# Kernel tuning notes

Hardware: AMD Instinct MI355X
Metric: run time of the kernel (lower is better)

Reference implementation:

```python
import jax, jax.numpy as jnp
from jax import lax
import numpy as np

B, T, IN, H, L = 64, 512, 256, 512, 2


def setup_inputs() -> dict:
    key = jax.random.key(0)
    k = jax.random.split(key, 5)
    s_w = 1.0 / np.sqrt(IN)
    s_u = 1.0 / np.sqrt(H)
    return {
        "x": jax.random.normal(k[0], (B, T, IN), dtype=jnp.float32),
        "W": jax.random.uniform(k[1], (3 * H, IN), dtype=jnp.float32, minval=-s_w, maxval=s_w),
        "b_W": jax.random.uniform(k[2], (3 * H,), dtype=jnp.float32, minval=-s_w, maxval=s_w),
        "U": jax.random.uniform(k[3], (3 * H, H), dtype=jnp.float32, minval=-s_u, maxval=s_u),
        "b_U": jax.random.uniform(k[4], (3 * H,), dtype=jnp.float32, minval=-s_u, maxval=s_u),
        "num_layers": L,
    }


def _cell(xt, h, W, b_W, U, b_U):
    # xt: [B, IN], h: [B, H]
    xg = xt @ W.T + b_W          # [B, 3H]
    hg = h @ U.T + b_U           # [B, 3H]
    xr, xu, xn = jnp.split(xg, 3, axis=1)
    hr, hu, hn = jnp.split(hg, 3, axis=1)
    r = jax.nn.sigmoid(xr + hr)
    u = jax.nn.sigmoid(xu + hu)
    n = jnp.tanh(xn + r * hn)
    return u * h + (1.0 - u) * n


def reference(x, W, b_W, U, b_U, num_layers):
    b, t, _ = x.shape
    hdim = U.shape[1]

    def step(h, xt):
        hs = []
        for _ in range(num_layers):  # shared cell reapplied to same xt
            h = _cell(xt, h, W, b_W, U, b_U)
            hs.append(h)
        return h, jnp.stack(hs)      # [L, B, H]

    h0 = jnp.zeros((b, hdim), x.dtype)
    _, hs = lax.scan(step, h0, jnp.swapaxes(x, 0, 1))  # [T, L, B, H]
    return hs.reshape(t * num_layers, b, hdim)
```

## Files before the change

### kernel.cpp

```cpp
#include <hip/hip_runtime.h>
#include <stdint.h>

#define BB   64
#define TT   512
#define KIN  256
#define HH   512
#define JGN  16
#define BGN  4
#define NJ2  32
#define NB   16
#define XPAD 260

typedef short bf16x8 __attribute__((ext_vector_type(8)));
typedef float f32x4  __attribute__((ext_vector_type(4)));

union U16x8 { unsigned short s[8]; bf16x8 v; };
union FU    { float f; unsigned u; };

__device__ __forceinline__ unsigned short f2bf(float f){
  FU v; v.f = f;
  unsigned r = v.u + 0x7fffu + ((v.u >> 16) & 1u);
  return (unsigned short)(r >> 16);
}
__device__ __forceinline__ float bf2f(unsigned short s){
  FU v; v.u = ((unsigned)s) << 16; return v.f;
}
__device__ __forceinline__ bf16x8 cvt8(const float* p){
  float4 a = ((const float4*)p)[0];
  float4 b = ((const float4*)p)[1];
  float f[8] = {a.x,a.y,a.z,a.w,b.x,b.y,b.z,b.w};
  U16x8 h;
  #pragma unroll
  for(int i=0;i<8;i++) h.s[i] = f2bf(f[i]);
  return h.v;
}
__device__ __forceinline__ void split8(const float* p, bf16x8& hi, bf16x8& lo){
  float4 a = ((const float4*)p)[0];
  float4 b = ((const float4*)p)[1];
  float f[8] = {a.x,a.y,a.z,a.w,b.x,b.y,b.z,b.w};
  U16x8 h,l;
  #pragma unroll
  for(int i=0;i<8;i++){
    unsigned short hb = f2bf(f[i]);
    l.s[i] = f2bf(f[i] - bf2f(hb));
    h.s[i] = hb;
  }
  hi = h.v; lo = l.v;
}
__device__ __forceinline__ void unpackg(uint4 A, uint4 B, bf16x8& hi, bf16x8& lo){
  unsigned wv[8] = {A.x,A.y,A.z,A.w,B.x,B.y,B.z,B.w};
  U16x8 h,l;
  #pragma unroll
  for(int j=0;j<8;j++){
    h.s[j] = (unsigned short)(wv[j] >> 16);
    l.s[j] = (unsigned short)(wv[j] & 0xffffu);
  }
  hi = h.v; lo = l.v;
}

#define MFMA __builtin_amdgcn_mfma_f32_16x16x32_bf16

#define LD4W(Q0,Q1,Q2,Q3, BASE) \
  asm volatile( \
    "global_load_dwordx4 %0, %4, off sc1\n\t" \
    "global_load_dwordx4 %1, %4, off offset:16 sc1\n\t" \
    "global_load_dwordx4 %2, %4, off offset:128 sc1\n\t" \
    "global_load_dwordx4 %3, %4, off offset:144 sc1\n\t" \
    "s_waitcnt vmcnt(0)" \
    : "=&v"(Q0),"=&v"(Q1),"=&v"(Q2),"=&v"(Q3) \
    : "v"(BASE) : "memory")

__global__ __launch_bounds__(512, 1) void gru_scan(
    const float* __restrict__ x,  const float* __restrict__ Wm,
    const float* __restrict__ bW, const float* __restrict__ Um,
    const float* __restrict__ bU, float* __restrict__ out,
    unsigned* __restrict__ hbuf,  unsigned* __restrict__ flags)
{
  __shared__ f32x4 red [8][6][64];
  __shared__ f32x4 red2[8][6][64];
  __shared__ float xlds[NB][XPAD];

  const int tid  = threadIdx.x;
  const int u    = tid >> 6;
  const int lane = tid & 63;
  const int col  = lane & 15;
  const int lg   = lane >> 4;
  const int bid  = blockIdx.x;
  const int bg   = bid >> 4;
  const int jg   = bid & 15;
  const int j0   = jg * NJ2;
  const int b0g  = bg * NB;

  bf16x8 BU[6][2], BW[6];
  #pragma unroll
  for(int nt=0; nt<6; nt++){
    int rl   = nt*16 + col;
    int g    = rl >> 5, jj = rl & 31;
    int grow = g*HH + j0 + jj;
    #pragma unroll
    for(int ks=0; ks<2; ks++)
      BU[nt][ks] = cvt8(Um + (size_t)grow*HH + u*64 + ks*32 + lg*8);
    BW[nt] = cvt8(Wm + (size_t)grow*KIN + u*32 + lg*8);
  }

  float bsr, bsu, bwn, bun;
  {
    int r0 = j0 + (u & 1)*16 + col;
    bsr = bW[r0]      + bU[r0];
    bsu = bW[HH + r0] + bU[HH + r0];
    bwn = bW[2*HH + r0];
    bun = bU[2*HH + r0];
  }

  float hreg[4] = {0.f,0.f,0.f,0.f};

  auto stage_x = [&](int tt){
    #pragma unroll
    for(int i=0; i<2; i++){
      int bl = u*2 + i;
      const float* gp = x + ((size_t)(b0g + bl)*TT + tt)*KIN + lane*4;
      __builtin_amdgcn_global_load_lds(
        (const __attribute__((address_space(1))) unsigned*)(const void*)gp,
        (__attribute__((address_space(3))) unsigned*)(void*)&xlds[bl][0],
        16, 0, 0);
    }
  };

  auto pollw = [&](int tgt){
    const unsigned* fp = flags + bg*JGN + 2*u;
    while(true){
      unsigned f = __hip_atomic_load(&fp[lane & 1], __ATOMIC_RELAXED,
                                     __HIP_MEMORY_SCOPE_AGENT);
      if(__all((int)(f >= (unsigned)tgt))) break;
      __builtin_amdgcn_s_sleep(1);
    }
    __builtin_amdgcn_sched_barrier(0);
    asm volatile("" ::: "memory");
  };

  auto h_mfma = [&](const unsigned* hb){
    const void* a0 = (const char*)(hb + (size_t)(b0g + col)*HH + u*64 + lg*8);
    uint4 q0,q1,q2,q3;
    LD4W(q0,q1,q2,q3, a0);
    __builtin_amdgcn_sched_barrier(0);
    f32x4 Ch[6];
    #pragma unroll
    for(int nt=0;nt<6;nt++) Ch[nt]=(f32x4){0,0,0,0};
    {
      bf16x8 ah, al;
      unpackg(q0,q1,ah,al);
      #pragma unroll
      for(int nt=0; nt<6; nt++){
        Ch[nt] = MFMA(ah, BU[nt][0], Ch[nt], 0,0,0);
        Ch[nt] = MFMA(al, BU[nt][0], Ch[nt], 0,0,0);
      }
      unpackg(q2,q3,ah,al);
      #pragma unroll
      for(int nt=0; nt<6; nt++){
        Ch[nt] = MFMA(ah, BU[nt][1], Ch[nt], 0,0,0);
        Ch[nt] = MFMA(al, BU[nt][1], Ch[nt], 0,0,0);
      }
    }
    #pragma unroll
    for(int nt=0;nt<6;nt++) red[u][nt][lane] = Ch[nt];
  };

  auto xg_partials = [&](){
    f32x4 Cx[6];
    #pragma unroll
    for(int nt=0;nt<6;nt++) Cx[nt]=(f32x4){0,0,0,0};
    bf16x8 ah, al;
    split8(&xlds[col][u*32 + lg*8], ah, al);
    #pragma unroll
    for(int nt=0; nt<6; nt++){
      Cx[nt] = MFMA(ah, BW[nt], Cx[nt], 0,0,0);
      Cx[nt] = MFMA(al, BW[nt], Cx[nt], 0,0,0);
    }
    #pragma unroll
    for(int nt=0;nt<6;nt++) red2[u][nt][lane] = Cx[nt];
  };

  auto xg_reduce = [&](f32x4 (&xg)[3]){
    #pragma unroll
    for(int gi=0; gi<3; gi++){
      int nt = gi*2 + u;
      f32x4 s = red2[0][nt][lane];
      #pragma unroll
      for(int pw=1; pw<8; pw++) s += red2[pw][nt][lane];
      xg[gi] = s;
    }
  };

  auto gates = [&](unsigned* hw, const f32x4 (&xgf)[3], float (&on)[4]){
    f32x4 hg[3];
    #pragma unroll
    for(int gi=0; gi<3; gi++){
      int nt = gi*2 + u;
      f32x4 s = red[0][nt][lane];
      #pragma unroll
      for(int pw=1; pw<8; pw++) s += red[pw][nt][lane];
      hg[gi] = s;
    }
    #pragma unroll
    for(int r=0;r<4;r++){
      float pr = xgf[0][r] + hg[0][r] + bsr;
      float pu = xgf[1][r] + hg[1][r] + bsu;
      float rg = __builtin_amdgcn_rcpf(1.f + __expf(-pr));
      float ug = __builtin_amdgcn_rcpf(1.f + __expf(-pu));
      float hn = hg[2][r] + bun;
      float z  = xgf[2][r] + bwn + rg*hn;
      z = fminf(fmaxf(z, -15.f), 15.f);
      float e  = __expf(2.f*z);
      float nn = (e - 1.f) * __builtin_amdgcn_rcpf(e + 1.f);
      float hnew = ug*hreg[r] + (1.f - ug)*nn;
      hreg[r] = hnew;
      on[r]   = hnew;
      unsigned short h16 = f2bf(hnew);
      unsigned short l16 = f2bf(hnew - bf2f(h16));
      __hip_atomic_store(&hw[(size_t)(b0g + lg*4 + r)*HH + j0 + u*16 + col],
                         ((unsigned)h16 << 16) | (unsigned)l16,
                         __ATOMIC_RELAXED, __HIP_MEMORY_SCOPE_AGENT);
    }
  };

  auto out_store = [&](int cell, const float (&on)[4]){
    if(u < 2){
      #pragma unroll
      for(int r=0;r<4;r++)
        out[((size_t)cell*BB + b0g + lg*4 + r)*HH + j0 + u*16 + col] = on[r];
    }
  };

  unsigned* hb0 = hbuf;
  unsigned* hb1 = hbuf + (size_t)BB*HH;

  f32x4 xgf[3] = {(f32x4){0,0,0,0},(f32x4){0,0,0,0},(f32x4){0,0,0,0}};
  f32x4 xgn[3] = {(f32x4){0,0,0,0},(f32x4){0,0,0,0},(f32x4){0,0,0,0}};
  float on0[4] = {0,0,0,0}, on1[4] = {0,0,0,0};

  stage_x(0);
  __syncthreads();
  xg_partials();
  __syncthreads();
  if(u < 2) xg_reduce(xgf);
  stage_x(1);
  __syncthreads();

  for(int t=0; t<TT; t++){
    pollw(2*t);
    h_mfma(hb0);
    if(t+1 < TT) xg_partials();
    __syncthreads();
    if(u < 2) gates(hb1, xgf, on0);
    __syncthreads();
    if(tid == 0)
      __hip_atomic_store(&flags[bid & 63], (unsigned)(2*t) + 1u,
                         __ATOMIC_RELAXED, __HIP_MEMORY_SCOPE_AGENT);
    if(u < 2 && t+1 < TT) xg_reduce(xgn);
    out_store(2*t, on0);

    if(t+2 < TT) stage_x(t+2);
    pollw(2*t + 1);
    h_mfma(hb1);
    __syncthreads();
    if(u < 2) gates(hb0, xgf, on1);
    __syncthreads();
    if(tid == 0)
      __hip_atomic_store(&flags[bid & 63], (unsigned)(2*t) + 2u,
                         __ATOMIC_RELAXED, __HIP_MEMORY_SCOPE_AGENT);
    out_store(2*t + 1, on1);

    xgf[0] = xgn[0]; xgf[1] = xgn[1]; xgf[2] = xgn[2];
  }
}

extern "C" void kernel_launch(void* const* d_in, const int* in_sizes, int n_in,
                              void* d_out, int out_size, void* d_ws, size_t ws_size,
                              hipStream_t stream) {
  const float* x  = (const float*)d_in[0];
  const float* Wm = (const float*)d_in[1];
  const float* bW = (const float*)d_in[2];
  const float* Um = (const float*)d_in[3];
  const float* bU = (const float*)d_in[4];
  float* out = (float*)d_out;

  unsigned* hbuf  = (unsigned*)d_ws;
  unsigned* flags = (unsigned*)((char*)d_ws + 2*BB*HH*sizeof(unsigned));
  (void)hipMemsetAsync(d_ws, 0, 2*BB*HH*sizeof(unsigned) + 256, stream);

  gru_scan<<<BGN*JGN, 512, 0, stream>>>(x, Wm, bW, Um, bU, out, hbuf, flags);
}
```

Before: 3.445 ms.

## Spread gate reduction and elementwise work across all eight waves

Only two of the eight waves previously reduced the cross-wave MFMA partials and computed the gates, each handling four rows per lane. The LDS reduction buffers are transposed to a per-component scalar layout so all eight waves take part, each lane owning one output element. This shortens the serial critical path between the two barriers of every recurrent step. In exchange it issues more scalar LDS stores and more load instructions per reduction, and the hidden-state publish stores are spread across more waves.

```diff
diff --git a/kernel.cpp b/kernel.cpp
--- a/kernel.cpp
+++ b/kernel.cpp
@@ -76,8 +76,8 @@
     const float* __restrict__ bU, float* __restrict__ out,
     unsigned* __restrict__ hbuf,  unsigned* __restrict__ flags)
 {
-  __shared__ f32x4 red [8][6][64];
-  __shared__ f32x4 red2[8][6][64];
+  __shared__ float redT [8][6][4][64];
+  __shared__ float red2T[8][6][4][64];
   __shared__ float xlds[NB][XPAD];
 
   const int tid  = threadIdx.x;
@@ -85,6 +85,8 @@
   const int lane = tid & 63;
   const int col  = lane & 15;
   const int lg   = lane >> 4;
+  const int ri   = u >> 1;
+  const int p    = u & 1;
   const int bid  = blockIdx.x;
   const int bg   = bid >> 4;
   const int jg   = bid & 15;
@@ -105,14 +107,14 @@
 
   float bsr, bsu, bwn, bun;
   {
-    int r0 = j0 + (u & 1)*16 + col;
+    int r0 = j0 + p*16 + col;
     bsr = bW[r0]      + bU[r0];
     bsu = bW[HH + r0] + bU[HH + r0];
     bwn = bW[2*HH + r0];
     bun = bU[2*HH + r0];
   }
 
-  float hreg[4] = {0.f,0.f,0.f,0.f};
+  float hreg = 0.f;
 
   auto stage_x = [&](int tt){
     #pragma unroll
@@ -162,7 +164,10 @@
       }
     }
     #pragma unroll
-    for(int nt=0;nt<6;nt++) red[u][nt][lane] = Ch[nt];
+    for(int nt=0;nt<6;nt++)
+      #pragma unroll
+      for(int r=0;r<4;r++)
+        redT[u][nt][r][lane] = Ch[nt][r];
   };
 
   auto xg_partials = [&](){
@@ -177,72 +182,69 @@
       Cx[nt] = MFMA(al, BW[nt], Cx[nt], 0,0,0);
     }
     #pragma unroll
-    for(int nt=0;nt<6;nt++) red2[u][nt][lane] = Cx[nt];
-  };
-
-  auto xg_reduce = [&](f32x4 (&xg)[3]){
+    for(int nt=0;nt<6;nt++)
+      #pragma unroll
+      for(int r=0;r<4;r++)
+        red2T[u][nt][r][lane] = Cx[nt][r];
+  };
+
+  auto xg_reduce = [&](float (&xg)[3]){
     #pragma unroll
     for(int gi=0; gi<3; gi++){
-      int nt = gi*2 + u;
-      f32x4 s = red2[0][nt][lane];
-      #pragma unroll
-      for(int pw=1; pw<8; pw++) s += red2[pw][nt][lane];
-      xg[gi] = s;
-    }
-  };
-
-  auto gates = [&](unsigned* hw, const f32x4 (&xgf)[3], float (&on)[4]){
-    f32x4 hg[3];
+      int nt = gi*2 + p;
+      float s0 = red2T[0][nt][ri][lane] + red2T[1][nt][ri][lane];
+      float s1 = red2T[2][nt][ri][lane] + red2T[3][nt][ri][lane];
+      float s2 = red2T[4][nt][ri][lane] + red2T[5][nt][ri][lane];
+      float s3 = red2T[6][nt][ri][lane] + red2T[7][nt][ri][lane];
+      xg[gi] = (s0 + s1) + (s2 + s3);
+    }
+  };
+
+  auto gates = [&](unsigned* hw, const float (&xgf)[3], float& on){
+    float hg[3];
     #pragma unroll
     for(int gi=0; gi<3; gi++){
-      int nt = gi*2 + u;
-      f32x4 s = red[0][nt][lane];
-      #pragma unroll
-      for(int pw=1; pw<8; pw++) s += red[pw][nt][lane];
-      hg[gi] = s;
-    }
-    #pragma unroll
-    for(int r=0;r<4;r++){
-      float pr = xgf[0][r] + hg[0][r] + bsr;
-      float pu = xgf[1][r] + hg[1][r] + bsu;
-      float rg = __builtin_amdgcn_rcpf(1.f + __expf(-pr));
-      float ug = __builtin_amdgcn_rcpf(1.f + __expf(-pu));
-      float hn = hg[2][r] + bun;
-      float z  = xgf[2][r] + bwn + rg*hn;
-      z = fminf(fmaxf(z, -15.f), 15.f);
-      float e  = __expf(2.f*z);
-      float nn = (e - 1.f) * __builtin_amdgcn_rcpf(e + 1.f);
-      float hnew = ug*hreg[r] + (1.f - ug)*nn;
-      hreg[r] = hnew;
-      on[r]   = hnew;
-      unsigned short h16 = f2bf(hnew);
-      unsigned short l16 = f2bf(hnew - bf2f(h16));
-      __hip_atomic_store(&hw[(size_t)(b0g + lg*4 + r)*HH + j0 + u*16 + col],
-                         ((unsigned)h16 << 16) | (unsigned)l16,
-                         __ATOMIC_RELAXED, __HIP_MEMORY_SCOPE_AGENT);
-    }
-  };
-
-  auto out_store = [&](int cell, const float (&on)[4]){
-    if(u < 2){
-      #pragma unroll
-      for(int r=0;r<4;r++)
-        out[((size_t)cell*BB + b0g + lg*4 + r)*HH + j0 + u*16 + col] = on[r];
-    }
+      int nt = gi*2 + p;
+      float s0 = redT[0][nt][ri][lane] + redT[1][nt][ri][lane];
+      float s1 = redT[2][nt][ri][lane] + redT[3][nt][ri][lane];
+      float s2 = redT[4][nt][ri][lane] + redT[5][nt][ri][lane];
+      float s3 = redT[6][nt][ri][lane] + redT[7][nt][ri][lane];
+      hg[gi] = (s0 + s1) + (s2 + s3);
+    }
+    float pr = xgf[0] + hg[0] + bsr;
+    float pu = xgf[1] + hg[1] + bsu;
+    float rg = __builtin_amdgcn_rcpf(1.f + __expf(-pr));
+    float ug = __builtin_amdgcn_rcpf(1.f + __expf(-pu));
+    float hn = hg[2] + bun;
+    float z  = xgf[2] + bwn + rg*hn;
+    z = fminf(fmaxf(z, -15.f), 15.f);
+    float e  = __expf(2.f*z);
+    float nn = (e - 1.f) * __builtin_amdgcn_rcpf(e + 1.f);
+    float hnew = ug*hreg + (1.f - ug)*nn;
+    hreg = hnew;
+    on   = hnew;
+    unsigned short h16 = f2bf(hnew);
+    unsigned short l16 = f2bf(hnew - bf2f(h16));
+    __hip_atomic_store(&hw[(size_t)(b0g + lg*4 + ri)*HH + j0 + p*16 + col],
+                       ((unsigned)h16 << 16) | (unsigned)l16,
+                       __ATOMIC_RELAXED, __HIP_MEMORY_SCOPE_AGENT);
+  };
+
+  auto out_store = [&](int cell, float on){
+    out[((size_t)cell*BB + b0g + lg*4 + ri)*HH + j0 + p*16 + col] = on;
   };
 
   unsigned* hb0 = hbuf;
   unsigned* hb1 = hbuf + (size_t)BB*HH;
 
-  f32x4 xgf[3] = {(f32x4){0,0,0,0},(f32x4){0,0,0,0},(f32x4){0,0,0,0}};
-  f32x4 xgn[3] = {(f32x4){0,0,0,0},(f32x4){0,0,0,0},(f32x4){0,0,0,0}};
-  float on0[4] = {0,0,0,0}, on1[4] = {0,0,0,0};
+  float xgf[3] = {0,0,0}, xgn[3] = {0,0,0};
+  float on0 = 0.f, on1 = 0.f;
 
   stage_x(0);
   __syncthreads();
   xg_partials();
   __syncthreads();
-  if(u < 2) xg_reduce(xgf);
+  xg_reduce(xgf);
   stage_x(1);
   __syncthreads();
 
@@ -251,19 +253,19 @@
     h_mfma(hb0);
     if(t+1 < TT) xg_partials();
     __syncthreads();
-    if(u < 2) gates(hb1, xgf, on0);
+    gates(hb1, xgf, on0);
     __syncthreads();
     if(tid == 0)
       __hip_atomic_store(&flags[bid & 63], (unsigned)(2*t) + 1u,
                          __ATOMIC_RELAXED, __HIP_MEMORY_SCOPE_AGENT);
-    if(u < 2 && t+1 < TT) xg_reduce(xgn);
+    if(t+1 < TT) xg_reduce(xgn);
     out_store(2*t, on0);
 
     if(t+2 < TT) stage_x(t+2);
     pollw(2*t + 1);
     h_mfma(hb1);
     __syncthreads();
-    if(u < 2) gates(hb0, xgf, on1);
+    gates(hb0, xgf, on1);
     __syncthreads();
     if(tid == 0)
       __hip_atomic_store(&flags[bid & 63], (unsigned)(2*t) + 2u,
```

Measured after the change: 3.106 ms, median of 2. 9.8% less time.
